# Optimization experiments

Hardware: AMD Instinct MI355X
Metric: run time of the kernel (lower is better)

## Reference

```python
import jax, jax.numpy as jnp
import numpy as np

DZ = 16
DX = 16
T = 256
LOG2PI = float(np.log(2.0 * np.pi))


def _cst(dim, det):
    # -0.5 * (dim*log(2*pi) + log|cov|)  (log-Gaussian normalizing constant)
    return -0.5 * (dim * LOG2PI + jnp.log(det))


def _kalman_update(pm, pc, y, H, d, R):
    S = H @ pc @ H.T + R
    K = pc @ H.T @ jnp.linalg.inv(S)
    m = pm + K @ (y - H @ pm - d)
    c = (jnp.eye(pc.shape[0], dtype=pc.dtype) - K @ H) @ pc
    return m, c


def _forward(observations, p_prior_mean, p_prior_cov, p_trans_w, p_trans_b,
             p_trans_cov, p_emis_w, p_emis_b, p_emis_cov,
             q_prior_mean, q_prior_cov, q_trans_w, q_trans_b, q_trans_cov,
             q_emis_w, q_emis_b, q_emis_cov):
    Tn, dx = observations.shape
    dz = p_trans_cov.shape[0]
    dt = observations.dtype
    I_z = jnp.eye(dz, dtype=dt)

    p_trans_prec = jnp.linalg.inv(p_trans_cov)
    p_trans_det = jnp.linalg.det(p_trans_cov)
    p_emis_prec = jnp.linalg.inv(p_emis_cov)
    p_emis_det = jnp.linalg.det(p_emis_cov)
    q_trans_prec = jnp.linalg.inv(q_trans_cov)

    # ---- t = 0 : init filtering (Kalman under q) and V terms ----
    fm, fc = _kalman_update(q_prior_mean, q_prior_cov, observations[0],
                            q_emis_w, q_emis_b, q_emis_cov)
    constants = _cst(dz, jnp.linalg.det(p_prior_cov)) + _cst(dx, p_emis_det)

    # quad-form term buffers; slot i becomes valid once appended at step i
    transOmega = jnp.broadcast_to(-0.5 * p_trans_prec, (Tn, dz, dz)).at[0].set(
        -0.5 * jnp.linalg.inv(p_prior_cov))
    obsOmega = -0.5 * p_emis_prec  # shared by every obs term
    transA = jnp.zeros((Tn, dz, dz), dt).at[0].set(I_z)
    transB = jnp.zeros((Tn, dz), dt).at[0].set(-p_prior_mean)
    obsA = jnp.zeros((Tn, dx, dz), dt).at[0].set(p_emis_w)
    obsB = jnp.zeros((Tn, dx), dt).at[0].set(p_emis_b - observations[0])

    idx = jnp.arange(Tn)

    def step(carry, inp):
        fm, fc, constants, transA, transB, obsA, obsB = carry
        y, t = inp
        mask = idx < t  # terms appended so far

        # backward kernel q(z_{t-1} | z_t) from current filtering law
        fprec = jnp.linalg.inv(fc)
        ct = q_trans_w.T @ q_trans_prec
        bcov = jnp.linalg.inv(ct @ q_trans_w + fprec)
        bA = bcov @ ct
        ba = bcov @ (fprec @ fm - ct @ q_trans_b)

        # filtering update (Kalman predict + correct under q)
        pm = q_trans_w @ fm + q_trans_b
        pc = q_trans_w @ fc @ q_trans_w.T + q_trans_cov
        fm2, fc2 = _kalman_update(pm, pc, y, q_emis_w, q_emis_b, q_emis_cov)

        # constants accumulated at this step
        c = constants + (_cst(dx, p_emis_det) + _cst(dz, p_trans_det)
                         - _cst(dz, jnp.linalg.det(bcov)) + 0.5 * dz
                         - 0.5 * jnp.trace(p_trans_prec @ p_trans_w @ bcov @ p_trans_w.T))
        # trace(Omega @ A @ bcov @ A.T) for every already-appended term
        c = c + jnp.sum(jnp.where(mask,
            jnp.einsum('tij,tjk,kl,til->t', transOmega, transA, bcov, transA), 0.0))
        c = c + jnp.sum(jnp.where(mask,
            jnp.einsum('ij,tjk,kl,til->t', obsOmega, obsA, bcov, obsA), 0.0))

        # integrate all existing quad forms under the backward kernel:
        # A <- A @ bA ; b <- A @ ba + b   (b uses the pre-update A)
        mA = mask[:, None, None]
        mb = mask[:, None]
        transB = jnp.where(mb, jnp.einsum('tij,j->ti', transA, ba) + transB, transB)
        transA = jnp.where(mA, jnp.einsum('tij,jk->tik', transA, bA), transA)
        obsB = jnp.where(mb, jnp.einsum('tij,j->ti', obsA, ba) + obsB, obsB)
        obsA = jnp.where(mA, jnp.einsum('tij,jk->tik', obsA, bA), obsA)

        # append the new transition and observation quad forms at slot t
        transA = transA.at[t].set(p_trans_w @ bA - I_z)
        transB = transB.at[t].set(p_trans_w @ ba + p_trans_b)
        obsA = obsA.at[t].set(p_emis_w)
        obsB = obsB.at[t].set(p_emis_b - y)

        return (fm2, fc2, c, transA, transB, obsA, obsB), None

    carry0 = (fm, fc, constants, transA, transB, obsA, obsB)
    (fm, fc, constants, transA, transB, obsA, obsB), _ = jax.lax.scan(
        step, carry0, (observations[1:], jnp.arange(1, Tn)))

    constants = constants - _cst(dz, jnp.linalg.det(fc))

    # expectation of every stored quad form under the final filtering law
    # (trace uses A @ cov @ A -- non-transposed, exactly as in the source)
    tr_t = jnp.einsum('tij,tjk,kl,tli->t', transOmega, transA, fc, transA)
    ct_t = jnp.einsum('tij,j->ti', transA, fm) + transB
    qf_t = jnp.einsum('ti,tij,tj->t', ct_t, transOmega, ct_t)
    tr_o = jnp.einsum('ij,tjk,kl,tli->t', obsOmega, obsA, fc, obsA)
    ct_o = jnp.einsum('tij,j->ti', obsA, fm) + obsB
    qf_o = jnp.einsum('ti,ij,tj->t', ct_o, obsOmega, ct_o)

    return constants + jnp.sum(tr_t + qf_t + tr_o + qf_o) + 0.5 * dz


def setup_inputs() -> dict:
    key = jax.random.key(0)
    ks = jax.random.split(key, 17)
    f32 = jnp.float32

    def cov(k, d):
        A = jax.random.normal(k, (d, d), f32) * 0.2
        return A @ A.T + jnp.eye(d, dtype=f32)  # SPD, well-conditioned

    def stable(k, d):
        return jax.random.normal(k, (d, d), f32) * (0.4 / np.sqrt(d))  # spectral norm < 1

    return dict(
        observations=jax.random.normal(ks[0], (T, DX), f32),
        p_prior_mean=jax.random.normal(ks[1], (DZ,), f32),
        p_prior_cov=cov(ks[2], DZ),
        p_trans_w=stable(ks[3], DZ),
        p_trans_b=jax.random.normal(ks[4], (DZ,), f32) * 0.1,
        p_trans_cov=cov(ks[5], DZ),
        p_emis_w=jax.random.normal(ks[6], (DX, DZ), f32) * (1.0 / np.sqrt(DZ)),
        p_emis_b=jax.random.normal(ks[7], (DX,), f32) * 0.1,
        p_emis_cov=cov(ks[8], DX),
        q_prior_mean=jax.random.normal(ks[9], (DZ,), f32),
        q_prior_cov=cov(ks[10], DZ),
        q_trans_w=stable(ks[11], DZ),
        q_trans_b=jax.random.normal(ks[12], (DZ,), f32) * 0.1,
        q_trans_cov=cov(ks[13], DZ),
        q_emis_w=jax.random.normal(ks[14], (DX, DZ), f32) * (1.0 / np.sqrt(DZ)),
        q_emis_b=jax.random.normal(ks[15], (DX,), f32) * 0.1,
        q_emis_cov=cov(ks[16], DX),
    )


def reference(observations, p_prior_mean, p_prior_cov, p_trans_w, p_trans_b,
              p_trans_cov, p_emis_w, p_emis_b, p_emis_cov,
              q_prior_mean, q_prior_cov, q_trans_w, q_trans_b, q_trans_cov,
              q_emis_w, q_emis_b, q_emis_cov):
    return _forward(observations, p_prior_mean, p_prior_cov, p_trans_w, p_trans_b,
                    p_trans_cov, p_emis_w, p_emis_b, p_emis_cov,
                    q_prior_mean, q_prior_cov, q_trans_w, q_trans_b, q_trans_cov,
                    q_emis_w, q_emis_b, q_emis_cov)
```

## Files before the change

kernel.cpp:

```cpp
#include <hip/hip_runtime.h>
#include <math.h>

#define L2P 1.8378770664093453f
#define TF 4
#define WUP 8

__device__ __forceinline__ void ld16(float* __restrict__ d, const float* __restrict__ p) {
  const float4 a = *(const float4*)(p);
  const float4 b = *(const float4*)(p + 4);
  const float4 cc = *(const float4*)(p + 8);
  const float4 e = *(const float4*)(p + 12);
  d[0] = a.x; d[1] = a.y; d[2] = a.z; d[3] = a.w;
  d[4] = b.x; d[5] = b.y; d[6] = b.z; d[7] = b.w;
  d[8] = cc.x; d[9] = cc.y; d[10] = cc.z; d[11] = cc.w;
  d[12] = e.x; d[13] = e.y; d[14] = e.z; d[15] = e.w;
}

__device__ __forceinline__ float dot16rr(const float* __restrict__ a,
                                         const float* __restrict__ b) {
  float s0 = 0.f, s1 = 0.f;
#pragma unroll
  for (int k = 0; k < 16; k += 2) {
    s0 = fmaf(a[k], b[k], s0);
    s1 = fmaf(a[k + 1], b[k + 1], s1);
  }
  return s0 + s1;
}

__device__ __forceinline__ float dotshfl16(const float* __restrict__ a, float v) {
  float s0 = 0.f, s1 = 0.f;
#pragma unroll
  for (int k = 0; k < 16; k += 2) {
    s0 = fmaf(a[k], __shfl(v, k, 16), s0);
    s1 = fmaf(a[k + 1], __shfl(v, k + 1, 16), s1);
  }
  return s0 + s1;
}

__device__ __forceinline__ float gj8_phase(const float* __restrict__ X,
                                           float* __restrict__ Y, int k, int tid) {
  const int rr0 = tid >> 5;
  const int ca = tid & 31;
  float p[8][8];
#pragma unroll
  for (int i = 0; i < 8; ++i) {
    const float4 v0 = *(const float4*)&X[(k + i) * 32 + k];
    const float4 v1 = *(const float4*)&X[(k + i) * 32 + k + 4];
    p[i][0] = v0.x; p[i][1] = v0.y; p[i][2] = v0.z; p[i][3] = v0.w;
    p[i][4] = v1.x; p[i][5] = v1.y; p[i][6] = v1.z; p[i][7] = v1.w;
  }
  float rhs[8];
#pragma unroll
  for (int i = 0; i < 8; ++i) rhs[i] = X[(k + i) * 32 + ca];
  float det = 1.f;
#pragma unroll
  for (int i = 0; i < 8; ++i) {
    det *= p[i][i];
    const float ip = __builtin_amdgcn_rcpf(p[i][i]);
#pragma unroll
    for (int j = i + 1; j < 8; ++j) p[i][j] *= ip;
    rhs[i] *= ip;
#pragma unroll
    for (int m2 = i + 1; m2 < 8; ++m2) {
      const float f = p[m2][i];
#pragma unroll
      for (int j = i + 1; j < 8; ++j) p[m2][j] = fmaf(-f, p[i][j], p[m2][j]);
      rhs[m2] = fmaf(-f, rhs[i], rhs[m2]);
    }
  }
  float w[8];
#pragma unroll
  for (int i = 7; i >= 0; --i) {
    float s = rhs[i];
#pragma unroll
    for (int j = i + 1; j < 8; ++j) s = fmaf(-p[i][j], w[j], s);
    w[i] = s;
  }
#pragma unroll
  for (int h = 0; h < 2; ++h) {
    const int rr = rr0 + 8 * h;
    float o;
    if (rr >= k && rr < k + 8) {
      o = w[rr - k];
    } else {
      const float4 s0 = *(const float4*)&X[rr * 32 + k];
      const float4 s1 = *(const float4*)&X[rr * 32 + k + 4];
      o = X[rr * 32 + ca] -
          (s0.x * w[0] + s0.y * w[1] + s0.z * w[2] + s0.w * w[3] +
           s1.x * w[4] + s1.y * w[5] + s1.z * w[6] + s1.w * w[7]);
    }
    Y[rr * 32 + ca] = o;
  }
  return det;
}

__device__ __forceinline__ float gjw_phase(const float* __restrict__ X,
                                           float* __restrict__ Y, int k, int lane) {
  const int ca = lane & 31;
  const int r8 = (lane >> 5) * 8;
  float p[8][8];
#pragma unroll
  for (int i = 0; i < 8; ++i) {
    const float4 v0 = *(const float4*)&X[(k + i) * 32 + k];
    const float4 v1 = *(const float4*)&X[(k + i) * 32 + k + 4];
    p[i][0] = v0.x; p[i][1] = v0.y; p[i][2] = v0.z; p[i][3] = v0.w;
    p[i][4] = v1.x; p[i][5] = v1.y; p[i][6] = v1.z; p[i][7] = v1.w;
  }
  float rhs[8];
#pragma unroll
  for (int i = 0; i < 8; ++i) rhs[i] = X[(k + i) * 32 + ca];
  float det = 1.f;
#pragma unroll
  for (int i = 0; i < 8; ++i) {
    det *= p[i][i];
    const float ip = __builtin_amdgcn_rcpf(p[i][i]);
#pragma unroll
    for (int j = i + 1; j < 8; ++j) p[i][j] *= ip;
    rhs[i] *= ip;
#pragma unroll
    for (int m2 = i + 1; m2 < 8; ++m2) {
      const float f = p[m2][i];
#pragma unroll
      for (int j = i + 1; j < 8; ++j) p[m2][j] = fmaf(-f, p[i][j], p[m2][j]);
      rhs[m2] = fmaf(-f, rhs[i], rhs[m2]);
    }
  }
  float w[8];
#pragma unroll
  for (int i = 7; i >= 0; --i) {
    float s = rhs[i];
#pragma unroll
    for (int j = i + 1; j < 8; ++j) s = fmaf(-p[i][j], w[j], s);
    w[i] = s;
  }
#pragma unroll
  for (int h = 0; h < 8; ++h) {
    const int rr = r8 + h;
    float o;
    if (rr >= k && rr < k + 8) {
      o = w[rr - k];
    } else {
      const float4 s0 = *(const float4*)&X[rr * 32 + k];
      const float4 s1 = *(const float4*)&X[rr * 32 + k + 4];
      o = X[rr * 32 + ca] -
          (s0.x * w[0] + s0.y * w[1] + s0.z * w[2] + s0.w * w[3] +
           s1.x * w[4] + s1.y * w[5] + s1.z * w[6] + s1.w * w[7]);
    }
    Y[rr * 32 + ca] = o;
  }
  return det;
}

__device__ __forceinline__ float gjw_store(const float* __restrict__ X,
                                           float* __restrict__ dst, float scale,
                                           int lane) {
  const int ca = lane & 31;
  const int r8 = (lane >> 5) * 8;
  float p[8][8];
#pragma unroll
  for (int i = 0; i < 8; ++i) {
    const float4 v0 = *(const float4*)&X[(8 + i) * 32 + 8];
    const float4 v1 = *(const float4*)&X[(8 + i) * 32 + 12];
    p[i][0] = v0.x; p[i][1] = v0.y; p[i][2] = v0.z; p[i][3] = v0.w;
    p[i][4] = v1.x; p[i][5] = v1.y; p[i][6] = v1.z; p[i][7] = v1.w;
  }
  float rhs[8];
#pragma unroll
  for (int i = 0; i < 8; ++i) rhs[i] = X[(8 + i) * 32 + ca];
  float det = 1.f;
#pragma unroll
  for (int i = 0; i < 8; ++i) {
    det *= p[i][i];
    const float ip = __builtin_amdgcn_rcpf(p[i][i]);
#pragma unroll
    for (int j = i + 1; j < 8; ++j) p[i][j] *= ip;
    rhs[i] *= ip;
#pragma unroll
    for (int m2 = i + 1; m2 < 8; ++m2) {
      const float f = p[m2][i];
#pragma unroll
      for (int j = i + 1; j < 8; ++j) p[m2][j] = fmaf(-f, p[i][j], p[m2][j]);
      rhs[m2] = fmaf(-f, rhs[i], rhs[m2]);
    }
  }
  float w[8];
#pragma unroll
  for (int i = 7; i >= 0; --i) {
    float s = rhs[i];
#pragma unroll
    for (int j = i + 1; j < 8; ++j) s = fmaf(-p[i][j], w[j], s);
    w[i] = s;
  }
  const bool st = (ca >= 16);
  const int cd = ca - 16;
#pragma unroll
  for (int h = 0; h < 8; ++h) {
    const int rr = r8 + h;
    float o;
    if (rr >= 8) {
      o = w[rr - 8];
    } else {
      const float4 s0 = *(const float4*)&X[rr * 32 + 8];
      const float4 s1 = *(const float4*)&X[rr * 32 + 12];
      o = X[rr * 32 + ca] -
          (s0.x * w[0] + s0.y * w[1] + s0.z * w[2] + s0.w * w[3] +
           s1.x * w[4] + s1.y * w[5] + s1.z * w[6] + s1.w * w[7]);
    }
    if (st) dst[rr * 16 + cd] = scale * o;
  }
  return det;
}

extern "C" __global__ __launch_bounds__(512, 1) void lgq_kernel(
    const float* __restrict__ g_obs, const float* __restrict__ g_ppm,
    const float* __restrict__ g_ppc, const float* __restrict__ g_ptw,
    const float* __restrict__ g_ptb, const float* __restrict__ g_ptc,
    const float* __restrict__ g_pew, const float* __restrict__ g_peb,
    const float* __restrict__ g_pec, const float* __restrict__ g_qpm,
    const float* __restrict__ g_qpc, const float* __restrict__ g_qtw,
    const float* __restrict__ g_qtb, const float* __restrict__ g_qtc,
    const float* __restrict__ g_qew, const float* __restrict__ g_qeb,
    const float* __restrict__ g_qec, float* __restrict__ out) {
  const int tid = threadIdx.x;
  const bool lo = tid < 256;
  const int t8 = tid & 255;
  const int r = t8 >> 4, c = tid & 15;
  const int hf = tid >> 8;
  const int wv = tid >> 6;
  const int lane = tid & 63;

  __shared__ __align__(16) float obs_s[4096];
  __shared__ __align__(16) float hyb[4096];
  __shared__ __align__(16) float eoy[4096];
  __shared__ float qOmO[256];
  __shared__ float ring[32];
  __shared__ __align__(16) float augA[512], augB[512];
  __shared__ __align__(16) float fcInv[256];
  __shared__ __align__(16) float Wq[256], Hq[256], Wp[256], We[256];
  __shared__ __align__(16) float qtp[256], Rinv[256], Qp0i[256];
  __shared__ __align__(16) float ct[256], M0[256], Eq[256], Eo[256], c3m[256];
  __shared__ __align__(16) float OmT[256], OmO[256], Om0[256];
  __shared__ __align__(16) float F0[256], W2n[256], Tt[256];
  __shared__ __align__(16) float S0[256], S1[256];
  __shared__ __align__(16) float bAT[320], t1T[320], Emat[256], fprec[256];
  __shared__ __align__(16) float bcovS[256], bAfN[256], A0fN[256], A0fT[320];
  __shared__ __align__(16) float ctT[320], WeT[320], Dm[256];
  __shared__ __align__(16) float R1m[256], R1T[320], R2m[256], R2T[320];
  __shared__ __align__(16) float T1m[256], T2m[256];
  __shared__ __align__(16) float BkA[256], BkAT[320], BkB[256], BkBT[320];
  __shared__ __align__(16) float hA256[256], hB256[256];
  __shared__ __align__(16) float eta[16], ba[16], u_t[16], zv[16];
  __shared__ __align__(16) float gb0[16], gb1[16], fm[16];
  __shared__ __align__(16) float etaF[16], gfin[16];
  __shared__ float qtb[16], dqv[16], ptb[16], peb[16], ppmv[16], qpmv[16];
  __shared__ float v0[16], u0[16], wc_s[16], uc_s[16], vta[16], bau0v[16];
  __shared__ float scl[8];
  __shared__ float cB_s;

  float* aug6A = hyb;
  float* aug6B = eoy;

#pragma unroll
  for (int j = 0; j < 8; ++j) obs_s[tid + 512 * j] = g_obs[tid + 512 * j];

  float trace_acc = 0.f, hacc = 0.f;

  if (wv < 6) {
    const float* M = (wv == 0) ? g_ptc : (wv == 1) ? g_pec : (wv == 2) ? g_qtc
                     : (wv == 3) ? g_qec : (wv == 4) ? g_ppc : g_qpc;
    float* A = aug6A + wv * 512;
    float* Bp = aug6B + wv * 512;
    const int ca = lane & 31;
    const int r8 = (lane >> 5) * 8;
#pragma unroll
    for (int h = 0; h < 8; ++h) {
      const int rr = r8 + h;
      A[rr * 32 + ca] = (ca < 16) ? M[rr * 16 + ca] : ((rr == ca - 16) ? 1.f : 0.f);
    }
    const float d0 = gjw_phase(A, Bp, 0, lane);
    float* dst = (wv == 0) ? OmT : (wv == 1) ? OmO : (wv == 2) ? qtp
                 : (wv == 3) ? Rinv : (wv == 4) ? Om0 : Qp0i;
    const float scale = (wv == 2 || wv == 3 || wv == 5) ? 1.0f : -0.5f;
    const float d1 = gjw_store(Bp, dst, scale, lane);
    if (lane == 0) { ring[wv * 2] = d0; ring[wv * 2 + 1] = d1; }
  } else if (wv == 6) {
    if (lane < 16) {
      qtb[lane] = g_qtb[lane];
      dqv[lane] = g_qeb[lane];
      ptb[lane] = g_ptb[lane];
      peb[lane] = g_peb[lane];
    } else if (lane < 32) {
      const int i = lane - 16;
      ppmv[i] = g_ppm[i];
      qpmv[i] = g_qpm[i];
    }
  } else {
#pragma unroll
    for (int j = 0; j < 4; ++j) {
      const int i = lane + 64 * j;
      Wq[i] = g_qtw[i];
      Hq[i] = g_qew[i];
      Wp[i] = g_ptw[i];
      We[i] = g_pew[i];
    }
  }

  __syncthreads();
  if (!hf) {
    float a = 0.f, b = 0.f;
#pragma unroll
    for (int k = 0; k < 16; ++k) {
      a = fmaf(Wq[k * 16 + r], qtp[k * 16 + c], a);
      b = fmaf(Hq[k * 16 + r], Rinv[k * 16 + c], b);
    }
    ct[t8] = a;
    Eq[t8] = b;
  } else {
    float d = 0.f, e = 0.f;
#pragma unroll
    for (int k = 0; k < 16; ++k) {
      d = fmaf(OmT[r * 16 + k], Wp[k * 16 + c], d);
      e = fmaf(We[k * 16 + r], OmO[k * 16 + c], e);
    }
    Tt[t8] = d;
    Eo[t8] = e;
  }

  __syncthreads();
  {
    float ym[16], ob[16];
#pragma unroll
    for (int k = 0; k < 16; ++k) {
      const float y = obs_s[t8 * 16 + k];
      ym[k] = y - dqv[k];
      ob[k] = peb[k] - y;
    }
    const int i0 = hf * 8;
#pragma unroll
    for (int i2 = 0; i2 < 8; ++i2) {
      const int i = i0 + i2;
      float a = 0.f, b = 0.f;
#pragma unroll
      for (int k = 0; k < 16; ++k) {
        a = fmaf(Eq[i * 16 + k], ym[k], a);
        b = fmaf(Eo[i * 16 + k], ob[k], b);
      }
      hyb[t8 * 16 + i] = a;
      eoy[t8 * 16 + i] = b;
    }
    if (hf) {
      float q = 0.f;
#pragma unroll
      for (int i = 0; i < 16; ++i) {
        float d = 0.f;
#pragma unroll
        for (int k = 0; k < 16; ++k) d = fmaf(OmO[i * 16 + k], ob[k], d);
        q = fmaf(ob[i], d, q);
      }
      qOmO[t8] = q;
    }
  }
  if (!hf) {
    float a = 0.f, b = 0.f;
#pragma unroll
    for (int k = 0; k < 16; ++k) {
      a = fmaf(ct[r * 16 + k], Wq[k * 16 + c], a);
      b = fmaf(Eq[r * 16 + k], Hq[k * 16 + c], b);
    }
    M0[t8] = a;
    F0[t8] = qtp[t8] + b;
    fprec[t8] = Qp0i[t8] + b;
    if (tid < 16) {
      float s = 0.f;
#pragma unroll
      for (int k = 0; k < 16; ++k) s = fmaf(ct[tid * 16 + k], qtb[k], s);
      u0[tid] = s;
    } else if (tid < 32) {
      const int i = tid - 16;
      float s = 0.f;
#pragma unroll
      for (int k = 0; k < 16; ++k) s = fmaf(qtp[i * 16 + k], qtb[k], s);
      v0[i] = s;
    } else if (tid < 48) {
      const int i = tid - 32;
      float s = 0.f;
#pragma unroll
      for (int k = 0; k < 16; ++k) s = fmaf(Om0[i * 16 + k], ppmv[k], s);
      vta[i] = s;
    } else if (tid < 64) {
      const int i = tid - 48;
      float s = 0.f;
#pragma unroll
      for (int k = 0; k < 16; ++k) s = fmaf(Tt[k * 16 + i], ptb[k], s);
      wc_s[i] = s;
    } else if (tid < 80) {
      const int i = tid - 64;
      float s = 0.f;
#pragma unroll
      for (int k = 0; k < 16; ++k) s = fmaf(OmT[i * 16 + k], ptb[k], s);
      uc_s[i] = s;
    }
  } else {
    float e = 0.f, co = 0.f;
#pragma unroll
    for (int k = 0; k < 16; ++k) {
      e = fmaf(Wp[k * 16 + r], Tt[k * 16 + c], e);
      co = fmaf(Eo[r * 16 + k], We[k * 16 + c], co);
    }
    W2n[t8] = e;
    S0[t8] = Om0[t8] + co + e;
    c3m[t8] = OmT[t8] + co + e;
  }

  float ct_c[16], ct_r[16], tt_r[16], wp_r[16];
  float f0_rc, d0_rc, c3_rc;
  __syncthreads();
  if (lo) {
    if (tid < 16) {
      float s = hyb[tid];
#pragma unroll
      for (int k = 0; k < 16; ++k) s = fmaf(Qp0i[tid * 16 + k], qpmv[k], s);
      eta[tid] = s;
      hacc += ppmv[tid] * vta[tid];
    } else if (tid < 32) {
      const int i = tid - 16;
      gb0[i] = eoy[i] - vta[i];
    }
    if (tid == 0) {
      float s = 0.f;
#pragma unroll
      for (int k = 0; k < 16; ++k) s = fmaf(ptb[k], uc_s[k], s);
      cB_s = s;
      hacc += qOmO[0];
    }
#pragma unroll
    for (int k = 0; k < 16; ++k) {
      ct_c[k] = ct[k * 16 + c];
      ct_r[k] = ct[k * 16 + r];
      tt_r[k] = Tt[r * 16 + k];
      wp_r[k] = Wp[r * 16 + k];
    }
    f0_rc = F0[tid];
    d0_rc = M0[tid] + F0[tid];
    c3_rc = c3m[tid];
    augA[r * 32 + c] = M0[tid] + fprec[tid];
    augA[r * 32 + 16 + c] = (r == c) ? 1.f : 0.f;
  }

  float* Scur = S0;
  float* Snxt = S1;
  float* gcur = gb0;
  float* gnxt = gb1;

#pragma unroll 1
  for (int t = 1; t <= TF; ++t) {
    const int rb = 12 + (t - 1) * 2;
    float sw_rc;
    __syncthreads();
    if (lo) {
      const float det = gj8_phase(augA, augB, 0, tid);
      if (tid == 0) ring[rb + 0] = det;
    } else if (wv == 4 && t > 1) {
      const int ec = lane & 15, er0 = lane >> 4;
      float t1c[16]; ld16(t1c, &t1T[ec * 20]);
#pragma unroll
      for (int q = 0; q < 4; ++q) {
        const int er = er0 + 4 * q;
        const int e = er * 16 + ec;
        float btr[16]; ld16(btr, &bAT[er * 20]);
        Snxt[e] = dot16rr(btr, t1c) - Emat[er * 16 + ec] - Emat[ec * 16 + er] + c3m[e];
      }
    } else if (wv == 5 && t > 1) {
      if (lane < 16) {
        float bti[16]; ld16(bti, &bAT[lane * 20]);
        float zvv[16]; ld16(zvv, zv);
        gnxt[lane] = -u_t[lane] + eoy[(t - 1) * 16 + lane] + dot16rr(bti, zvv);
      }
    }
    if (t > 1) {
      float* tp = Scur; Scur = Snxt; Snxt = tp;
      tp = gcur; gcur = gnxt; gnxt = tp;
    }
    __syncthreads();
    if (lo) {
      const float det = gj8_phase(augB, augA, 8, tid);
      if (tid == 0) ring[rb + 1] = det;
    }
    __syncthreads();
    if (lo) {
      float brow[16]; ld16(brow, &augA[r * 32 + 16]);
      const float acc = dot16rr(brow, ct_c);
      bAT[c * 20 + r] = acc;
      const float bce = augA[r * 32 + 16 + c];
      if (t == TF) { bAfN[tid] = acc; bcovS[tid] = bce; }
      sw_rc = Scur[tid];
      trace_acc = fmaf(bce, sw_rc, trace_acc);
      if (tid < 16) {
        float bc[16]; ld16(bc, &augA[tid * 32 + 16]);
        float a2 = 0.f;
#pragma unroll
        for (int k = 0; k < 16; ++k) a2 = fmaf(bc[k], eta[k] - u0[k], a2);
        ba[tid] = a2;
      }
    }
    __syncthreads();
    if (lo) {
      float bcol[16]; ld16(bcol, &bAT[c * 20]);
      float swr[16];  ld16(swr, &Scur[r * 16]);
      float a1 = 0.f, ae = 0.f, af = 0.f;
#pragma unroll
      for (int k = 0; k < 16; ++k) {
        a1 = fmaf(swr[k], bcol[k], a1);
        ae = fmaf(tt_r[k], bcol[k], ae);
        af = fmaf(ct_r[k], bcol[k], af);
      }
      t1T[c * 20 + r] = a1;
      Emat[tid] = ae;
      fprec[tid] = f0_rc - af;
      augA[r * 32 + c] = d0_rc - af;
      augA[r * 32 + 16 + c] = (r == c) ? 1.f : 0.f;
      if (t == TF) {
        float a0 = 0.f;
#pragma unroll
        for (int k = 0; k < 16; ++k) a0 = fmaf(wp_r[k], bcol[k], a0);
        a0 -= (r == c) ? 1.f : 0.f;
        A0fN[tid] = a0;
        A0fT[c * 20 + r] = a0;
      }
      const float bar = ba[r], bac = ba[c];
      hacc = fmaf(bar * sw_rc, bac, hacc);
      if (r == 0) hacc += 2.f * bac * (gcur[c] + wc_s[c]);
      if (tid == 0) hacc += cB_s + qOmO[t];
    } else if (wv == 5) {
      if (lane < 16) {
        const int i = lane;
        float e = v0[i] + hyb[t * 16 + i];
#pragma unroll
        for (int k = 0; k < 16; ++k) e = fmaf(ct[k * 16 + i], ba[k], e);
        eta[i] = e;
      } else if (lane < 32) {
        const int i = lane - 16;
        float ttrow[16]; ld16(ttrow, &Tt[i * 16]);
        float bav[16]; ld16(bav, ba);
        u_t[i] = uc_s[i] + dot16rr(ttrow, bav);
      } else if (lane < 48) {
        const int i = lane - 32;
        float swrow[16]; ld16(swrow, &Scur[i * 16]);
        float bav[16]; ld16(bav, ba);
        zv[i] = gcur[i] + wc_s[i] + dot16rr(swrow, bav);
      }
    } else if (wv == 6 && t == TF) {
      if (lane < 16) {
        float bc[16]; ld16(bc, &bcovS[lane * 16]);
        float u0v[16]; ld16(u0v, u0);
        bau0v[lane] = dot16rr(bc, u0v);
      }
    }
  }

  __syncthreads();
  if (lo) {
    float btr[16]; ld16(btr, &bAT[r * 20]);
    float t1c[16]; ld16(t1c, &t1T[c * 20]);
    Snxt[tid] = dot16rr(btr, t1c) - Emat[r * 16 + c] - Emat[c * 16 + r] + c3_rc;
    float bcr[16]; ld16(bcr, &bcovS[r * 16]);
    float ctrow[16]; ld16(ctrow, &ct[c * 16]);
    Dm[tid] = dot16rr(bcr, ctrow);
    ctT[c * 20 + r] = ct[tid];
    WeT[c * 20 + r] = We[tid];
  } else {
    float tmp[16];
#pragma unroll
    for (int k = 0; k < 16; ++k) tmp[k] = v0[k] + hyb[t8 * 16 + k];
#pragma unroll
    for (int i = 0; i < 16; ++i) {
      float s = -bau0v[i];
#pragma unroll
      for (int k = 0; k < 16; ++k) s = fmaf(bcovS[i * 16 + k], tmp[k], s);
      obs_s[t8 * 16 + i] = s;
    }
    if (t8 >= TF) {
#pragma unroll
      for (int i = 0; i < 16; ++i) eoy[t8 * 16 + i] -= uc_s[i];
    }
  }
  { float* tp = Scur; Scur = Snxt; Snxt = tp; }

  __syncthreads();
  if (lo) {
    const int grp = tid >> 4;
    const int i = tid & 15;
    float drow[16], swr[16], ttr[16], bcol[16];
    ld16(drow, &Dm[i * 16]);
    ld16(swr, &Scur[i * 16]);
    ld16(ttr, &Tt[i * 16]);
    ld16(bcol, &bAT[i * 20]);
    const float wci = wc_s[i];
    float ba_p, zv_p;
    if (grp == 0) {
      ba_p = ba[i]; zv_p = zv[i];
    } else {
      ba_p = 0.f; zv_p = 0.f;
    }
    float haccA = 0.f, haccB = 0.f;
    const int tstart = (TF + 1) + grp * 16 - WUP;
#pragma unroll 1
    for (int j = 0; j < WUP + 16; ++j) {
      if (grp == 0 && j < WUP) continue;
      const int t = tstart + j;
      const int trd = (t > 255) ? 255 : t;
      const float w_c = obs_s[(trd - 1) * 16 + i];
      const float eu_c = eoy[(trd - 1) * 16 + i];
      const float ban = dotshfl16(drow, ba_p) + w_c;
      const float q = dotshfl16(ttr, ba_p);
      const float bz = dotshfl16(bcol, zv_p);
      const float gnew = eu_c - q + bz;
      const float ssw = dotshfl16(swr, ban);
      if (j >= WUP && t <= 255) {
        haccA = fmaf(ban, ssw, haccA);
        haccB = fmaf(ban, gnew + wci, haccB);
      }
      if (t <= 255) {
        zv_p = gnew + wci + ssw;
        ba_p = ban;
      }
    }
    hA256[tid] = haccA;
    hB256[tid] = haccB;
    if (grp == 15) {
      const float eu_c = eoy[255 * 16 + i];
      gfin[i] = eu_c - dotshfl16(ttr, ba_p) + dotshfl16(bcol, zv_p);
      float ctcol[16]; ld16(ctcol, &ctT[i * 20]);
      etaF[i] = v0[i] + hyb[255 * 16 + i] + dotshfl16(ctcol, ba_p);
    }
  } else if (wv == 4) {
    const int ca = lane & 31;
    const int r8 = (lane >> 5) * 8;
#pragma unroll
    for (int h = 0; h < 8; ++h) {
      const int rr = r8 + h;
      augA[rr * 32 + ca] = (ca < 16) ? fprec[rr * 16 + ca] : ((rr == ca - 16) ? 1.f : 0.f);
    }
    const float d0 = gjw_phase(augA, augB, 0, lane);
    const float d1 = gjw_store(augB, fcInv, 1.0f, lane);
    if (lane == 0) { ring[12 + TF * 2] = d0; ring[12 + TF * 2 + 1] = d1; }
  } else if (wv == 5) {
    const int ec = lane & 15, er0 = lane >> 4;
    {
      float a0c[16]; ld16(a0c, &A0fT[ec * 20]);
      float wec[16]; ld16(wec, &WeT[ec * 20]);
#pragma unroll
      for (int q = 0; q < 4; ++q) {
        const int er = er0 + 4 * q;
        const int e = er * 16 + ec;
        float omtr[16]; ld16(omtr, &OmT[er * 16]);
        float omor[16]; ld16(omor, &OmO[er * 16]);
        const float c1 = dot16rr(omtr, a0c);
        R1m[e] = c1; R1T[ec * 20 + er] = c1;
        const float c2 = dot16rr(omor, wec);
        R2m[e] = c2; R2T[ec * 20 + er] = c2;
        BkA[e] = bAfN[e];
        BkAT[ec * 20 + er] = bAT[ec * 20 + er];
      }
    }
    float* pBk = BkA;  float* pBkT = BkAT;
    float* pBn = BkB;  float* pBnT = BkBT;
#pragma unroll 1
    for (int it = 0; it < 4; ++it) {
      {
        float r1c[16]; ld16(r1c, &R1T[ec * 20]);
        float r2c[16]; ld16(r2c, &R2T[ec * 20]);
        float bkc[16]; ld16(bkc, &pBkT[ec * 20]);
#pragma unroll
        for (int q = 0; q < 4; ++q) {
          const int er = er0 + 4 * q;
          const int e = er * 16 + ec;
          float bkr[16]; ld16(bkr, &pBk[er * 16]);
          T1m[e] = dot16rr(bkr, r1c);
          T2m[e] = dot16rr(bkr, r2c);
          const float bsq = dot16rr(bkr, bkc);
          pBn[e] = bsq;
          pBnT[ec * 20 + er] = bsq;
        }
      }
      {
        float bkc[16]; ld16(bkc, &pBkT[ec * 20]);
#pragma unroll
        for (int q = 0; q < 4; ++q) {
          const int er = er0 + 4 * q;
          const int e = er * 16 + ec;
          float t1r[16]; ld16(t1r, &T1m[er * 16]);
          float t2r[16]; ld16(t2r, &T2m[er * 16]);
          const float n1 = R1m[e] + dot16rr(t1r, bkc);
          const float n2 = R2m[e] + dot16rr(t2r, bkc);
          R1m[e] = n1; R1T[ec * 20 + er] = n1;
          R2m[e] = n2; R2T[ec * 20 + er] = n2;
        }
      }
      { float* tp = pBk; pBk = pBn; pBn = tp; }
      { float* tp = pBkT; pBkT = pBnT; pBnT = tp; }
    }
  }

  __syncthreads();
  if (tid < 16) {
    float fr[16]; ld16(fr, &fcInv[tid * 16]);
    float ev[16]; ld16(ev, etaF);
    fm[tid] = dot16rr(fr, ev);
  }
  __syncthreads();

  {
    float psum = 0.f;
    if (lo) {
      const float cnt = 255.f - (float)TF;
      psum = trace_acc + hacc;
      psum += cnt * bcovS[tid] * Scur[tid];
      {
        float a0rowc[16]; ld16(a0rowc, &A0fN[c * 16]);
        float r1colr[16]; ld16(r1colr, &R1T[r * 20]);
        float werowc[16]; ld16(werowc, &We[c * 16]);
        float r2colr[16]; ld16(r2colr, &R2T[r * 20]);
        const float zcr = dot16rr(a0rowc, r1colr) + dot16rr(werowc, r2colr);
        psum += fcInv[tid] * zcr;
      }
      psum += fm[r] * (Scur[tid] - W2n[tid]) * fm[c];
      if (r == 0) psum += 2.f * fm[c] * gfin[c];
      psum += hA256[tid] + 2.f * hB256[tid];
      if (tid > TF) psum += qOmO[tid];
      if (tid == 0) psum += cnt * cB_s;
#pragma unroll 1
      for (int i = tid; i < 12 + TF * 2 + 2; i += 256) {
        float w;
        if (i < 2) w = 255.f;
        else if (i < 4) w = 256.f;
        else if (i < 8) w = 0.f;
        else if (i < 10) w = 1.f;
        else if (i < 12) w = 0.f;
        else if (i < 12 + TF * 2) w = (i >= 12 + (TF - 1) * 2) ? (1.f + cnt) : 1.f;
        else w = 1.f;
        if (w != 0.f) psum -= 0.5f * w * logf(ring[i]);
      }
    }
#pragma unroll
    for (int off = 32; off; off >>= 1) psum += __shfl_down(psum, off, 64);
    if ((tid & 63) == 0) scl[tid >> 6] = psum;
  }
  __syncthreads();
  if (tid == 0) {
    const float base = -16.f * L2P + 255.f * (8.f - 8.f * L2P) + 8.f * L2P + 8.f;
    out[0] = scl[0] + scl[1] + scl[2] + scl[3] + scl[4] + scl[5] + scl[6] + scl[7] + base;
  }
}

extern "C" void kernel_launch(void* const* d_in, const int* in_sizes, int n_in,
                              void* d_out, int out_size, void* d_ws, size_t ws_size,
                              hipStream_t stream) {
  (void)in_sizes; (void)n_in; (void)out_size; (void)d_ws; (void)ws_size;
  lgq_kernel<<<1, 512, 0, stream>>>(
      (const float*)d_in[0], (const float*)d_in[1], (const float*)d_in[2],
      (const float*)d_in[3], (const float*)d_in[4], (const float*)d_in[5],
      (const float*)d_in[6], (const float*)d_in[7], (const float*)d_in[8],
      (const float*)d_in[9], (const float*)d_in[10], (const float*)d_in[11],
      (const float*)d_in[12], (const float*)d_in[13], (const float*)d_in[14],
      (const float*)d_in[15], (const float*)d_in[16], (float*)d_out);
}
```

Baseline: 127.5 us.

## Remove barriers by keeping setup values in registers and deferring small scalar work

```diff
diff --git a/kernel.cpp b/kernel.cpp
--- a/kernel.cpp
+++ b/kernel.cpp
@@ -238,9 +238,9 @@
   __shared__ __align__(16) float fcInv[256];
   __shared__ __align__(16) float Wq[256], Hq[256], Wp[256], We[256];
   __shared__ __align__(16) float qtp[256], Rinv[256], Qp0i[256];
-  __shared__ __align__(16) float ct[256], M0[256], Eq[256], Eo[256], c3m[256];
+  __shared__ __align__(16) float ct[256], Eq[256], Eo[256], c3m[256];
   __shared__ __align__(16) float OmT[256], OmO[256], Om0[256];
-  __shared__ __align__(16) float F0[256], W2n[256], Tt[256];
+  __shared__ __align__(16) float W2n[256], Tt[256];
   __shared__ __align__(16) float S0[256], S1[256];
   __shared__ __align__(16) float bAT[320], t1T[320], Emat[256], fprec[256];
   __shared__ __align__(16) float bcovS[256], bAfN[256], A0fN[256], A0fT[320];
@@ -250,7 +250,7 @@
   __shared__ __align__(16) float BkA[256], BkAT[320], BkB[256], BkBT[320];
   __shared__ __align__(16) float hA256[256], hB256[256];
   __shared__ __align__(16) float eta[16], ba[16], u_t[16], zv[16];
-  __shared__ __align__(16) float gb0[16], gb1[16], fm[16];
+  __shared__ __align__(16) float gb0[16], gb1[16];
   __shared__ __align__(16) float etaF[16], gfin[16];
   __shared__ float qtb[16], dqv[16], ptb[16], peb[16], ppmv[16], qpmv[16];
   __shared__ float v0[16], u0[16], wc_s[16], uc_s[16], vta[16], bau0v[16];
@@ -326,6 +326,8 @@
     Eo[t8] = e;
   }
 
+  float ct_c[16], ct_r[16], tt_r[16], wp_r[16];
+  float f0_rc, d0_rc;
   __syncthreads();
   {
     float ym[16], ob[16];
@@ -367,9 +369,9 @@
       a = fmaf(ct[r * 16 + k], Wq[k * 16 + c], a);
       b = fmaf(Eq[r * 16 + k], Hq[k * 16 + c], b);
     }
-    M0[t8] = a;
-    F0[t8] = qtp[t8] + b;
-    fprec[t8] = Qp0i[t8] + b;
+    const float f0v = qtp[t8] + b;
+    const float fpv = Qp0i[t8] + b;
+    fprec[t8] = fpv;
     if (tid < 16) {
       float s = 0.f;
 #pragma unroll
@@ -391,47 +393,14 @@
       const int i = tid - 48;
       float s = 0.f;
 #pragma unroll
-      for (int k = 0; k < 16; ++k) s = fmaf(Tt[k * 16 + i], ptb[k], s);
-      wc_s[i] = s;
+      for (int k = 0; k < 16; ++k) s = fmaf(OmT[i * 16 + k], ptb[k], s);
+      uc_s[i] = s;
     } else if (tid < 80) {
       const int i = tid - 64;
       float s = 0.f;
 #pragma unroll
-      for (int k = 0; k < 16; ++k) s = fmaf(OmT[i * 16 + k], ptb[k], s);
-      uc_s[i] = s;
-    }
-  } else {
-    float e = 0.f, co = 0.f;
-#pragma unroll
-    for (int k = 0; k < 16; ++k) {
-      e = fmaf(Wp[k * 16 + r], Tt[k * 16 + c], e);
-      co = fmaf(Eo[r * 16 + k], We[k * 16 + c], co);
-    }
-    W2n[t8] = e;
-    S0[t8] = Om0[t8] + co + e;
-    c3m[t8] = OmT[t8] + co + e;
-  }
-
-  float ct_c[16], ct_r[16], tt_r[16], wp_r[16];
-  float f0_rc, d0_rc, c3_rc;
-  __syncthreads();
-  if (lo) {
-    if (tid < 16) {
-      float s = hyb[tid];
-#pragma unroll
-      for (int k = 0; k < 16; ++k) s = fmaf(Qp0i[tid * 16 + k], qpmv[k], s);
-      eta[tid] = s;
-      hacc += ppmv[tid] * vta[tid];
-    } else if (tid < 32) {
-      const int i = tid - 16;
-      gb0[i] = eoy[i] - vta[i];
-    }
-    if (tid == 0) {
-      float s = 0.f;
-#pragma unroll
-      for (int k = 0; k < 16; ++k) s = fmaf(ptb[k], uc_s[k], s);
-      cB_s = s;
-      hacc += qOmO[0];
+      for (int k = 0; k < 16; ++k) s = fmaf(Tt[k * 16 + i], ptb[k], s);
+      wc_s[i] = s;
     }
 #pragma unroll
     for (int k = 0; k < 16; ++k) {
@@ -440,11 +409,20 @@
       tt_r[k] = Tt[r * 16 + k];
       wp_r[k] = Wp[r * 16 + k];
     }
-    f0_rc = F0[tid];
-    d0_rc = M0[tid] + F0[tid];
-    c3_rc = c3m[tid];
-    augA[r * 32 + c] = M0[tid] + fprec[tid];
+    f0_rc = f0v;
+    d0_rc = a + f0v;
+    augA[r * 32 + c] = a + fpv;
     augA[r * 32 + 16 + c] = (r == c) ? 1.f : 0.f;
+  } else {
+    float e = 0.f, co = 0.f;
+#pragma unroll
+    for (int k = 0; k < 16; ++k) {
+      e = fmaf(Wp[k * 16 + r], Tt[k * 16 + c], e);
+      co = fmaf(Eo[r * 16 + k], We[k * 16 + c], co);
+    }
+    W2n[t8] = e;
+    S0[t8] = Om0[t8] + co + e;
+    c3m[t8] = OmT[t8] + co + e;
   }
 
   float* Scur = S0;
@@ -455,7 +433,6 @@
 #pragma unroll 1
   for (int t = 1; t <= TF; ++t) {
     const int rb = 12 + (t - 1) * 2;
-    float sw_rc;
     __syncthreads();
     if (lo) {
       const float det = gj8_phase(augA, augB, 0, tid);
@@ -470,11 +447,30 @@
         float btr[16]; ld16(btr, &bAT[er * 20]);
         Snxt[e] = dot16rr(btr, t1c) - Emat[er * 16 + ec] - Emat[ec * 16 + er] + c3m[e];
       }
-    } else if (wv == 5 && t > 1) {
-      if (lane < 16) {
-        float bti[16]; ld16(bti, &bAT[lane * 20]);
-        float zvv[16]; ld16(zvv, zv);
-        gnxt[lane] = -u_t[lane] + eoy[(t - 1) * 16 + lane] + dot16rr(bti, zvv);
+    } else if (wv == 5) {
+      if (t > 1) {
+        if (lane < 16) {
+          float bti[16]; ld16(bti, &bAT[lane * 20]);
+          float zvv[16]; ld16(zvv, zv);
+          gnxt[lane] = -u_t[lane] + eoy[(t - 1) * 16 + lane] + dot16rr(bti, zvv);
+        }
+      } else {
+        if (lane < 16) {
+          float s = hyb[lane];
+#pragma unroll
+          for (int k = 0; k < 16; ++k) s = fmaf(Qp0i[lane * 16 + k], qpmv[k], s);
+          eta[lane] = s;
+        } else if (lane < 32) {
+          const int i = lane - 16;
+          gb0[i] = eoy[i] - vta[i];
+        }
+      }
+    } else if (wv == 6 && t == 1) {
+      if (lane == 0) {
+        float s = 0.f;
+#pragma unroll
+        for (int k = 0; k < 16; ++k) s = fmaf(ptb[k], uc_s[k], s);
+        cB_s = s;
       }
     }
     if (t > 1) {
@@ -485,28 +481,26 @@
     if (lo) {
       const float det = gj8_phase(augB, augA, 8, tid);
       if (tid == 0) ring[rb + 1] = det;
-    }
-    __syncthreads();
-    if (lo) {
-      float brow[16]; ld16(brow, &augA[r * 32 + 16]);
+      const int wrow = ((wv & 3) << 1) + ((lane >> 4) & 1) + ((lane >> 5) << 3);
+      const int qc = lane & 15;
+      float brow[16]; ld16(brow, &augA[wrow * 32 + 16]);
       const float acc = dot16rr(brow, ct_c);
-      bAT[c * 20 + r] = acc;
-      const float bce = augA[r * 32 + 16 + c];
-      if (t == TF) { bAfN[tid] = acc; bcovS[tid] = bce; }
-      sw_rc = Scur[tid];
-      trace_acc = fmaf(bce, sw_rc, trace_acc);
-      if (tid < 16) {
-        float bc[16]; ld16(bc, &augA[tid * 32 + 16]);
+      bAT[qc * 20 + wrow] = acc;
+      const float bce = brow[qc];
+      trace_acc = fmaf(bce, Scur[wrow * 16 + qc], trace_acc);
+      if (t == TF) { bAfN[wrow * 16 + qc] = acc; bcovS[wrow * 16 + qc] = bce; }
+      if (qc == 0) {
         float a2 = 0.f;
 #pragma unroll
-        for (int k = 0; k < 16; ++k) a2 = fmaf(bc[k], eta[k] - u0[k], a2);
-        ba[tid] = a2;
+        for (int k = 0; k < 16; ++k) a2 = fmaf(brow[k], eta[k] - u0[k], a2);
+        ba[wrow] = a2;
       }
     }
     __syncthreads();
     if (lo) {
       float bcol[16]; ld16(bcol, &bAT[c * 20]);
       float swr[16];  ld16(swr, &Scur[r * 16]);
+      const float sw_rc = swr[c];
       float a1 = 0.f, ae = 0.f, af = 0.f;
 #pragma unroll
       for (int k = 0; k < 16; ++k) {
@@ -562,7 +556,7 @@
   if (lo) {
     float btr[16]; ld16(btr, &bAT[r * 20]);
     float t1c[16]; ld16(t1c, &t1T[c * 20]);
-    Snxt[tid] = dot16rr(btr, t1c) - Emat[r * 16 + c] - Emat[c * 16 + r] + c3_rc;
+    Snxt[tid] = dot16rr(btr, t1c) - Emat[r * 16 + c] - Emat[c * 16 + r] + c3m[tid];
     float bcr[16]; ld16(bcr, &bcovS[r * 16]);
     float ctrow[16]; ld16(ctrow, &ct[c * 16]);
     Dm[tid] = dot16rr(bcr, ctrow);
@@ -703,13 +697,6 @@
   }
 
   __syncthreads();
-  if (tid < 16) {
-    float fr[16]; ld16(fr, &fcInv[tid * 16]);
-    float ev[16]; ld16(ev, etaF);
-    fm[tid] = dot16rr(fr, ev);
-  }
-  __syncthreads();
-
   {
     float psum = 0.f;
     if (lo) {
@@ -724,10 +711,18 @@
         const float zcr = dot16rr(a0rowc, r1colr) + dot16rr(werowc, r2colr);
         psum += fcInv[tid] * zcr;
       }
-      psum += fm[r] * (Scur[tid] - W2n[tid]) * fm[c];
-      if (r == 0) psum += 2.f * fm[c] * gfin[c];
+      {
+        float fcr[16]; ld16(fcr, &fcInv[r * 16]);
+        float fcc[16]; ld16(fcc, &fcInv[c * 16]);
+        float ev[16];  ld16(ev, etaF);
+        const float fmr = dot16rr(fcr, ev);
+        const float fmc = dot16rr(fcc, ev);
+        psum += fmr * (Scur[tid] - W2n[tid]) * fmc;
+        if (r == 0) psum += 2.f * fmc * gfin[c];
+      }
       psum += hA256[tid] + 2.f * hB256[tid];
-      if (tid > TF) psum += qOmO[tid];
+      if (tid < 16) psum += ppmv[tid] * vta[tid];
+      if (tid > TF || tid == 0) psum += qOmO[tid];
       if (tid == 0) psum += cnt * cB_s;
 #pragma unroll 1
       for (int i = tid; i < 12 + TF * 2 + 2; i += 256) {
```

Measured after the change: 121.8 us. 1.05x faster.
